# Optimization experiments

Measured on AMD Instinct MI355X. Metric: run time of the kernel, lower is better.

## Reference

```python
import jax, jax.numpy as jnp
import numpy as np

ITERS = 10
EPS = 1e-6
TEMPERATURE = 1.0


def setup_inputs() -> dict:
    key = jax.random.key(0)
    S, E = 524288, 64
    logits = jax.random.normal(key, (S, E), dtype=jnp.float32)
    return {"logits": logits, "top_k": 2}


def reference(logits, top_k):
    s, e = logits.shape
    scores = (logits / TEMPERATURE).astype(jnp.float32)
    scores = scores - jnp.max(scores, axis=-1, keepdims=True)
    q = jnp.exp(scores)
    col_target = float(s) / float(max(e, 1))

    def body(q, _):
        q = q / (jnp.sum(q, axis=1, keepdims=True) + EPS)
        q = q / (jnp.sum(q, axis=0, keepdims=True) + EPS) * col_target
        return q, None

    q, _ = jax.lax.scan(body, q, None, length=ITERS)
    q = q / (jnp.sum(q, axis=1, keepdims=True) + EPS)
    vals, idx = jax.lax.top_k(q, top_k)
    w = vals / (jnp.sum(vals, axis=-1, keepdims=True) + EPS)
    return idx.astype(jnp.int64), w.astype(logits.dtype)
```

## Files before the change

kernel.cpp:

```cpp
#include <hip/hip_runtime.h>
#include <math.h>

#define EPS 1e-6f
#define NE 64
#define THREADS 256
#define WPB 4
#define NBLOCKS 1024
#define ITERS 10

template <int ctrl>
__device__ __forceinline__ float dppf(float x) {
    return __int_as_float(__builtin_amdgcn_update_dpp(
        0, __float_as_int(x), ctrl, 0xf, 0xf, true));
}
template <int ctrl>
__device__ __forceinline__ int dppi(int x) {
    return __builtin_amdgcn_update_dpp(0, x, ctrl, 0xf, 0xf, true);
}

__device__ __forceinline__ float group16_sum(float v) {
    v += dppf<0xB1>(v);
    v += dppf<0x4E>(v);
    v += dppf<0x141>(v);
    v += dppf<0x140>(v);
    return v;
}

#define ARGMAX_STEP(CTRL)                                      \
    {                                                          \
        float ov = dppf<CTRL>(v);                              \
        int oi = dppi<CTRL>(i);                                \
        if (ov > v || (ov == v && oi < i)) { v = ov; i = oi; } \
    }

__device__ __forceinline__ void group16_argmax(float& v, int& i) {
    ARGMAX_STEP(0xB1)
    ARGMAX_STEP(0x4E)
    ARGMAX_STEP(0x141)
    ARGMAX_STEP(0x140)
}

__global__ void sink_init(float* __restrict__ r, float* __restrict__ c, int S) {
    int i = blockIdx.x * blockDim.x + threadIdx.x;
    if (i < S) r[i] = 1.0f;
    if (i < NE) c[i] = 1.0f;
}

__global__ __launch_bounds__(THREADS) void sink_pass(
    const float4* __restrict__ logits4, float* __restrict__ r,
    const float* __restrict__ c, float* __restrict__ Pblk, int nquads) {
    const int lane = threadIdx.x & 63;
    const int wib = threadIdx.x >> 6;
    const int g = lane >> 4;
    const int h = lane & 15;

    const float4 c4 = ((const float4*)c)[h];

    float4 pacc = {0.f, 0.f, 0.f, 0.f};
    int wave = blockIdx.x * WPB + wib;
    int nw = gridDim.x * WPB;

    for (int quad = wave; quad < nquads; quad += nw) {
        float4 v = logits4[(size_t)quad * 64 + lane];
        float4 q;
        q.x = __expf(v.x); q.y = __expf(v.y);
        q.z = __expf(v.z); q.w = __expf(v.w);
        float s = q.x * c4.x + q.y * c4.y + q.z * c4.z + q.w * c4.w;
        s = group16_sum(s);
        int row = quad * 4 + g;
        float rold = r[row];
        float rnew = rold / (rold * s + EPS);
        if (h == 0) r[row] = rnew;
        pacc.x += q.x * rnew; pacc.y += q.y * rnew;
        pacc.z += q.z * rnew; pacc.w += q.w * rnew;
    }

    __shared__ float4 plds[WPB][64];
    plds[wib][lane] = pacc;
    __syncthreads();
    if (threadIdx.x < NE) {
        int j = threadIdx.x;
        int hh = j >> 2, kk = j & 3;
        float t = 0.f;
#pragma unroll
        for (int w = 0; w < WPB; ++w)
#pragma unroll
            for (int gg = 0; gg < 4; ++gg) {
                const float* p = (const float*)&plds[w][gg * 16 + hh];
                t += p[kk];
            }
        Pblk[blockIdx.x * NE + j] = t;
    }
}

__global__ __launch_bounds__(1024) void sink_reduce(
    const float* __restrict__ Pblk, float* __restrict__ c, float col_target) {
    const int j = threadIdx.x & 63;
    const int chunk = threadIdx.x >> 6;
    const int per = NBLOCKS / 16;
    float t = 0.f;
    int b0 = chunk * per;
    for (int b = b0; b < b0 + per; ++b) t += Pblk[b * NE + j];
    __shared__ float lds[16][NE];
    lds[chunk][j] = t;
    __syncthreads();
    if (threadIdx.x < NE) {
        float P = 0.f;
#pragma unroll
        for (int k = 0; k < 16; ++k) P += lds[k][threadIdx.x];
        float cj = c[threadIdx.x];
        c[threadIdx.x] = cj * col_target / (cj * P + EPS);
    }
}

__global__ __launch_bounds__(THREADS) void sink_final(
    const float4* __restrict__ logits4, const float* __restrict__ r,
    const float* __restrict__ c, float2* __restrict__ oidx,
    float2* __restrict__ ow, int nquads) {
    const int lane = threadIdx.x & 63;
    const int wib = threadIdx.x >> 6;
    const int g = lane >> 4;
    const int h = lane & 15;
    const int base_col = h * 4;

    const float4 c4 = ((const float4*)c)[h];

    int wave = blockIdx.x * WPB + wib;
    int nw = gridDim.x * WPB;

    for (int quad = wave; quad < nquads; quad += nw) {
        float4 vv = logits4[(size_t)quad * 64 + lane];
        float4 u;
        u.x = __expf(vv.x) * c4.x; u.y = __expf(vv.y) * c4.y;
        u.z = __expf(vv.z) * c4.z; u.w = __expf(vv.w) * c4.w;
        float s = group16_sum(u.x + u.y + u.z + u.w);
        int row = quad * 4 + g;
        float rold = r[row];
        float rnew = rold / (rold * s + EPS);
        float4 val;
        val.x = u.x * rnew; val.y = u.y * rnew;
        val.z = u.z * rnew; val.w = u.w * rnew;

        float v = val.x; int i = base_col;
        if (val.y > v) { v = val.y; i = base_col + 1; }
        if (val.z > v) { v = val.z; i = base_col + 2; }
        if (val.w > v) { v = val.w; i = base_col + 3; }
        group16_argmax(v, i);
        float v1 = v; int i1 = i;

        float4 mv;
        mv.x = (i1 == base_col)     ? -INFINITY : val.x;
        mv.y = (i1 == base_col + 1) ? -INFINITY : val.y;
        mv.z = (i1 == base_col + 2) ? -INFINITY : val.z;
        mv.w = (i1 == base_col + 3) ? -INFINITY : val.w;
        v = mv.x; i = base_col;
        if (mv.y > v) { v = mv.y; i = base_col + 1; }
        if (mv.z > v) { v = mv.z; i = base_col + 2; }
        if (mv.w > v) { v = mv.w; i = base_col + 3; }
        group16_argmax(v, i);
        float v2 = v; int i2 = i;

        if (h == 0) {
            float wsum = v1 + v2 + EPS;
            oidx[row] = make_float2((float)i1, (float)i2);
            ow[row] = make_float2(v1 / wsum, v2 / wsum);
        }
    }
}

extern "C" void kernel_launch(void* const* d_in, const int* in_sizes, int n_in,
                              void* d_out, int out_size, void* d_ws, size_t ws_size,
                              hipStream_t stream) {
    const float* logits = (const float*)d_in[0];
    const int S = in_sizes[0] / NE;
    const int nquads = S / 4;
    const float col_target = (float)S / (float)NE;

    float* r = (float*)d_ws;
    float* c = r + S;
    float* Pblk = c + NE;

    float* out = (float*)d_out;
    float2* oidx = (float2*)out;
    float2* ow = (float2*)(out + (size_t)2 * S);

    sink_init<<<(S + THREADS - 1) / THREADS, THREADS, 0, stream>>>(r, c, S);
    for (int it = 0; it < ITERS; ++it) {
        sink_pass<<<NBLOCKS, THREADS, 0, stream>>>(
            (const float4*)logits, r, c, Pblk, nquads);
        sink_reduce<<<1, 1024, 0, stream>>>(Pblk, c, col_target);
    }
    sink_final<<<NBLOCKS, THREADS, 0, stream>>>(
        (const float4*)logits, r, c, oidx, ow, nquads);
}
```

Baseline: 602.3 us.

## Fuse Sinkhorn iterations into one persistent cooperative kernel with LDS-resident row scales

Replaces the 22 separate launches (init, pass/reduce per iteration, final) with one cooperative kernel of 256 blocks by 1024 threads. Blocks sync through grid.sync and a double-buffered partial column-sum array. Each wave owns a fixed contiguous range of rows, so the row scale factors stay in shared memory instead of global memory, and the next logits row is software-prefetched. This removes launch gaps and the global traffic for the r vector. In exchange, each block recomputes the 64-column reduction redundantly after every grid sync. It also assumes nquads divides evenly by NBLK*WPB and that each block's rows fit in MAXROWS; it does, since 512 quads per wave times 4 rows gives 2048. With only 256 blocks the logits streaming may get less memory-level parallelism.

```diff
diff --git a/kernel.cpp b/kernel.cpp
--- a/kernel.cpp
+++ b/kernel.cpp
@@ -1,12 +1,16 @@
 #include <hip/hip_runtime.h>
+#include <hip/hip_cooperative_groups.h>
 #include <math.h>
+
+namespace cg = cooperative_groups;
 
 #define EPS 1e-6f
 #define NE 64
-#define THREADS 256
-#define WPB 4
-#define NBLOCKS 1024
+#define NBLK 256
+#define TPB 1024
+#define WPB 16
 #define ITERS 10
+#define MAXROWS 2048
 
 template <int ctrl>
 __device__ __forceinline__ float dppf(float x) {
@@ -40,127 +44,132 @@
     ARGMAX_STEP(0x140)
 }
 
-__global__ void sink_init(float* __restrict__ r, float* __restrict__ c, int S) {
-    int i = blockIdx.x * blockDim.x + threadIdx.x;
-    if (i < S) r[i] = 1.0f;
-    if (i < NE) c[i] = 1.0f;
-}
-
-__global__ __launch_bounds__(THREADS) void sink_pass(
-    const float4* __restrict__ logits4, float* __restrict__ r,
-    const float* __restrict__ c, float* __restrict__ Pblk, int nquads) {
-    const int lane = threadIdx.x & 63;
-    const int wib = threadIdx.x >> 6;
+__global__ __launch_bounds__(TPB, 1) void sink_all(
+    const float4* __restrict__ logits4, float* __restrict__ Pblk,
+    float2* __restrict__ oidx, float2* __restrict__ ow, int nquads,
+    float col_target) {
+    cg::grid_group grid = cg::this_grid();
+    const int tid = threadIdx.x;
+    const int lane = tid & 63;
+    const int wib = tid >> 6;
     const int g = lane >> 4;
     const int h = lane & 15;
+    const int qpw = nquads / (NBLK * WPB);
+    const int qbase = (blockIdx.x * WPB + wib) * qpw;
 
-    const float4 c4 = ((const float4*)c)[h];
+    __shared__ float s_r[MAXROWS];
+    __shared__ float s_c[NE];
+    __shared__ float4 s_pl[WPB][64];
+    float* s_red = (float*)s_pl;
 
-    float4 pacc = {0.f, 0.f, 0.f, 0.f};
-    int wave = blockIdx.x * WPB + wib;
-    int nw = gridDim.x * WPB;
+    for (int i = tid; i < MAXROWS; i += TPB) s_r[i] = 1.0f;
+    if (tid < NE) s_c[tid] = 1.0f;
+    __syncthreads();
 
-    for (int quad = wave; quad < nquads; quad += nw) {
-        float4 v = logits4[(size_t)quad * 64 + lane];
-        float4 q;
-        q.x = __expf(v.x); q.y = __expf(v.y);
-        q.z = __expf(v.z); q.w = __expf(v.w);
-        float s = q.x * c4.x + q.y * c4.y + q.z * c4.z + q.w * c4.w;
-        s = group16_sum(s);
-        int row = quad * 4 + g;
-        float rold = r[row];
-        float rnew = rold / (rold * s + EPS);
-        if (h == 0) r[row] = rnew;
-        pacc.x += q.x * rnew; pacc.y += q.y * rnew;
-        pacc.z += q.z * rnew; pacc.w += q.w * rnew;
+    for (int it = 0; it < ITERS; ++it) {
+        float4 c4;
+        c4.x = s_c[h * 4 + 0]; c4.y = s_c[h * 4 + 1];
+        c4.z = s_c[h * 4 + 2]; c4.w = s_c[h * 4 + 3];
+
+        float4 pacc = {0.f, 0.f, 0.f, 0.f};
+        float4 v = logits4[(size_t)qbase * 64 + lane];
+        for (int k = 0; k < qpw; ++k) {
+            float4 cur = v;
+            if (k + 1 < qpw)
+                v = logits4[(size_t)(qbase + k + 1) * 64 + lane];
+            float4 q;
+            q.x = __expf(cur.x); q.y = __expf(cur.y);
+            q.z = __expf(cur.z); q.w = __expf(cur.w);
+            float s = q.x * c4.x + q.y * c4.y + q.z * c4.z + q.w * c4.w;
+            s = group16_sum(s);
+            int lrow = (wib * qpw + k) * 4 + g;
+            float rold = s_r[lrow];
+            float rnew = rold / (rold * s + EPS);
+            if (h == 0) s_r[lrow] = rnew;
+            pacc.x += q.x * rnew; pacc.y += q.y * rnew;
+            pacc.z += q.z * rnew; pacc.w += q.w * rnew;
+        }
+
+        __syncthreads();
+        s_pl[wib][lane] = pacc;
+        __syncthreads();
+        float* Pout = Pblk + (size_t)(it & 1) * NBLK * NE;
+        if (tid < NE) {
+            int j = tid, hh = j >> 2, kk = j & 3;
+            float t = 0.f;
+#pragma unroll
+            for (int w = 0; w < WPB; ++w)
+#pragma unroll
+                for (int gg = 0; gg < 4; ++gg)
+                    t += ((const float*)&s_pl[w][gg * 16 + hh])[kk];
+            Pout[blockIdx.x * NE + j] = t;
+        }
+        __threadfence();
+        grid.sync();
+
+        const float* Pin = Pblk + (size_t)(it & 1) * NBLK * NE;
+        {
+            int j = tid & 63;
+            int chunk = tid >> 6;
+            float t = 0.f;
+            int b0 = chunk * (NBLK / 16);
+            for (int b = b0; b < b0 + NBLK / 16; ++b) t += Pin[b * NE + j];
+            __syncthreads();
+            s_red[chunk * NE + j] = t;
+            __syncthreads();
+            if (tid < NE) {
+                float P = 0.f;
+#pragma unroll
+                for (int k = 0; k < 16; ++k) P += s_red[k * NE + tid];
+                float cj = s_c[tid];
+                s_c[tid] = cj * col_target / (cj * P + EPS);
+            }
+            __syncthreads();
+        }
     }
 
-    __shared__ float4 plds[WPB][64];
-    plds[wib][lane] = pacc;
-    __syncthreads();
-    if (threadIdx.x < NE) {
-        int j = threadIdx.x;
-        int hh = j >> 2, kk = j & 3;
-        float t = 0.f;
-#pragma unroll
-        for (int w = 0; w < WPB; ++w)
-#pragma unroll
-            for (int gg = 0; gg < 4; ++gg) {
-                const float* p = (const float*)&plds[w][gg * 16 + hh];
-                t += p[kk];
-            }
-        Pblk[blockIdx.x * NE + j] = t;
-    }
-}
-
-__global__ __launch_bounds__(1024) void sink_reduce(
-    const float* __restrict__ Pblk, float* __restrict__ c, float col_target) {
-    const int j = threadIdx.x & 63;
-    const int chunk = threadIdx.x >> 6;
-    const int per = NBLOCKS / 16;
-    float t = 0.f;
-    int b0 = chunk * per;
-    for (int b = b0; b < b0 + per; ++b) t += Pblk[b * NE + j];
-    __shared__ float lds[16][NE];
-    lds[chunk][j] = t;
-    __syncthreads();
-    if (threadIdx.x < NE) {
-        float P = 0.f;
-#pragma unroll
-        for (int k = 0; k < 16; ++k) P += lds[k][threadIdx.x];
-        float cj = c[threadIdx.x];
-        c[threadIdx.x] = cj * col_target / (cj * P + EPS);
-    }
-}
-
-__global__ __launch_bounds__(THREADS) void sink_final(
-    const float4* __restrict__ logits4, const float* __restrict__ r,
-    const float* __restrict__ c, float2* __restrict__ oidx,
-    float2* __restrict__ ow, int nquads) {
-    const int lane = threadIdx.x & 63;
-    const int wib = threadIdx.x >> 6;
-    const int g = lane >> 4;
-    const int h = lane & 15;
+    float4 c4;
+    c4.x = s_c[h * 4 + 0]; c4.y = s_c[h * 4 + 1];
+    c4.z = s_c[h * 4 + 2]; c4.w = s_c[h * 4 + 3];
     const int base_col = h * 4;
 
-    const float4 c4 = ((const float4*)c)[h];
-
-    int wave = blockIdx.x * WPB + wib;
-    int nw = gridDim.x * WPB;
-
-    for (int quad = wave; quad < nquads; quad += nw) {
-        float4 vv = logits4[(size_t)quad * 64 + lane];
+    float4 v = logits4[(size_t)qbase * 64 + lane];
+    for (int k = 0; k < qpw; ++k) {
+        float4 cur = v;
+        if (k + 1 < qpw)
+            v = logits4[(size_t)(qbase + k + 1) * 64 + lane];
         float4 u;
-        u.x = __expf(vv.x) * c4.x; u.y = __expf(vv.y) * c4.y;
-        u.z = __expf(vv.z) * c4.z; u.w = __expf(vv.w) * c4.w;
+        u.x = __expf(cur.x) * c4.x; u.y = __expf(cur.y) * c4.y;
+        u.z = __expf(cur.z) * c4.z; u.w = __expf(cur.w) * c4.w;
         float s = group16_sum(u.x + u.y + u.z + u.w);
-        int row = quad * 4 + g;
-        float rold = r[row];
+        int lrow = (wib * qpw + k) * 4 + g;
+        float rold = s_r[lrow];
         float rnew = rold / (rold * s + EPS);
         float4 val;
         val.x = u.x * rnew; val.y = u.y * rnew;
         val.z = u.z * rnew; val.w = u.w * rnew;
 
-        float v = val.x; int i = base_col;
-        if (val.y > v) { v = val.y; i = base_col + 1; }
-        if (val.z > v) { v = val.z; i = base_col + 2; }
-        if (val.w > v) { v = val.w; i = base_col + 3; }
-        group16_argmax(v, i);
-        float v1 = v; int i1 = i;
+        float vv = val.x; int i = base_col;
+        if (val.y > vv) { vv = val.y; i = base_col + 1; }
+        if (val.z > vv) { vv = val.z; i = base_col + 2; }
+        if (val.w > vv) { vv = val.w; i = base_col + 3; }
+        { float& v = vv; group16_argmax(v, i); }
+        float v1 = vv; int i1 = i;
 
         float4 mv;
         mv.x = (i1 == base_col)     ? -INFINITY : val.x;
         mv.y = (i1 == base_col + 1) ? -INFINITY : val.y;
         mv.z = (i1 == base_col + 2) ? -INFINITY : val.z;
         mv.w = (i1 == base_col + 3) ? -INFINITY : val.w;
-        v = mv.x; i = base_col;
-        if (mv.y > v) { v = mv.y; i = base_col + 1; }
-        if (mv.z > v) { v = mv.z; i = base_col + 2; }
-        if (mv.w > v) { v = mv.w; i = base_col + 3; }
-        group16_argmax(v, i);
-        float v2 = v; int i2 = i;
+        vv = mv.x; i = base_col;
+        if (mv.y > vv) { vv = mv.y; i = base_col + 1; }
+        if (mv.z > vv) { vv = mv.z; i = base_col + 2; }
+        if (mv.w > vv) { vv = mv.w; i = base_col + 3; }
+        { float& v = vv; group16_argmax(v, i); }
+        float v2 = vv; int i2 = i;
 
         if (h == 0) {
+            int row = (qbase + k) * 4 + g;
             float wsum = v1 + v2 + EPS;
             oidx[row] = make_float2((float)i1, (float)i2);
             ow[row] = make_float2(v1 / wsum, v2 / wsum);
@@ -173,23 +182,18 @@
                               hipStream_t stream) {
     const float* logits = (const float*)d_in[0];
     const int S = in_sizes[0] / NE;
-    const int nquads = S / 4;
-    const float col_target = (float)S / (float)NE;
+    int nquads = S / 4;
+    float col_target = (float)S / (float)NE;
 
-    float* r = (float*)d_ws;
-    float* c = r + S;
-    float* Pblk = c + NE;
+    float* Pblk = (float*)d_ws;
 
     float* out = (float*)d_out;
     float2* oidx = (float2*)out;
     float2* ow = (float2*)(out + (size_t)2 * S);
 
-    sink_init<<<(S + THREADS - 1) / THREADS, THREADS, 0, stream>>>(r, c, S);
-    for (int it = 0; it < ITERS; ++it) {
-        sink_pass<<<NBLOCKS, THREADS, 0, stream>>>(
-            (const float4*)logits, r, c, Pblk, nquads);
-        sink_reduce<<<1, 1024, 0, stream>>>(Pblk, c, col_target);
-    }
-    sink_final<<<NBLOCKS, THREADS, 0, stream>>>(
-        (const float4*)logits, r, c, oidx, ow, nquads);
+    const float4* logits4 = (const float4*)logits;
+    void* args[] = {(void*)&logits4, (void*)&Pblk, (void*)&oidx,
+                    (void*)&ow, (void*)&nquads, (void*)&col_target};
+    hipLaunchCooperativeKernel((void*)sink_all, dim3(NBLK), dim3(TPB), args,
+                               0, stream);
 }
```

Result: slower. 1.367 ms (+126.9%).

## Software-prefetch contiguous per-wave chunks and specialize first Sinkhorn pass

Applied to the files above, without the earlier changes.

Each wave now owns a contiguous run of quads instead of a grid-stride loop. Logits and r values are register double-buffered in groups of four quads, so the loads for the next group are in flight while the current group is computed. A templated FIRST pass assumes r and c are all ones, which lets the separate init kernel and the first r/c reads be dropped. The code assumes nquads divides evenly by waves times the prefetch depth, and it uses more registers.

```diff
diff --git a/kernel.cpp b/kernel.cpp
--- a/kernel.cpp
+++ b/kernel.cpp
@@ -6,7 +6,9 @@
 #define THREADS 256
 #define WPB 4
 #define NBLOCKS 1024
+#define NWAVES (NBLOCKS * WPB)
 #define ITERS 10
+#define PF 4
 
 template <int ctrl>
 __device__ __forceinline__ float dppf(float x) {
@@ -40,12 +42,7 @@
     ARGMAX_STEP(0x140)
 }
 
-__global__ void sink_init(float* __restrict__ r, float* __restrict__ c, int S) {
-    int i = blockIdx.x * blockDim.x + threadIdx.x;
-    if (i < S) r[i] = 1.0f;
-    if (i < NE) c[i] = 1.0f;
-}
-
+template <bool FIRST>
 __global__ __launch_bounds__(THREADS) void sink_pass(
     const float4* __restrict__ logits4, float* __restrict__ r,
     const float* __restrict__ c, float* __restrict__ Pblk, int nquads) {
@@ -53,26 +50,58 @@
     const int wib = threadIdx.x >> 6;
     const int g = lane >> 4;
     const int h = lane & 15;
-
-    const float4 c4 = ((const float4*)c)[h];
+    const int qpw = nquads / NWAVES;
+    const int qbase = (blockIdx.x * WPB + wib) * qpw;
+
+    float4 c4;
+    if (FIRST) c4 = make_float4(1.f, 1.f, 1.f, 1.f);
+    else       c4 = ((const float4*)c)[h];
+
+    const float4* lp = logits4 + (size_t)qbase * 64 + lane;
+
+    float4 buf[PF];
+    float rbuf[PF];
+#pragma unroll
+    for (int p = 0; p < PF; ++p) buf[p] = lp[(size_t)p * 64];
+    if (!FIRST) {
+#pragma unroll
+        for (int p = 0; p < PF; ++p) rbuf[p] = r[(qbase + p) * 4 + g];
+    }
 
     float4 pacc = {0.f, 0.f, 0.f, 0.f};
-    int wave = blockIdx.x * WPB + wib;
-    int nw = gridDim.x * WPB;
-
-    for (int quad = wave; quad < nquads; quad += nw) {
-        float4 v = logits4[(size_t)quad * 64 + lane];
-        float4 q;
-        q.x = __expf(v.x); q.y = __expf(v.y);
-        q.z = __expf(v.z); q.w = __expf(v.w);
-        float s = q.x * c4.x + q.y * c4.y + q.z * c4.z + q.w * c4.w;
-        s = group16_sum(s);
-        int row = quad * 4 + g;
-        float rold = r[row];
-        float rnew = rold / (rold * s + EPS);
-        if (h == 0) r[row] = rnew;
-        pacc.x += q.x * rnew; pacc.y += q.y * rnew;
-        pacc.z += q.z * rnew; pacc.w += q.w * rnew;
+    const int nb = qpw / PF;
+    for (int b = 0; b < nb; ++b) {
+        float4 cur[PF];
+        float rcur[PF];
+#pragma unroll
+        for (int p = 0; p < PF; ++p) {
+            cur[p] = buf[p];
+            if (!FIRST) rcur[p] = rbuf[p];
+        }
+        if (b + 1 < nb) {
+            const float4* np = lp + (size_t)(b + 1) * PF * 64;
+#pragma unroll
+            for (int p = 0; p < PF; ++p) buf[p] = np[(size_t)p * 64];
+            if (!FIRST) {
+#pragma unroll
+                for (int p = 0; p < PF; ++p)
+                    rbuf[p] = r[(qbase + (b + 1) * PF + p) * 4 + g];
+            }
+        }
+#pragma unroll
+        for (int p = 0; p < PF; ++p) {
+            float4 q;
+            q.x = __expf(cur[p].x); q.y = __expf(cur[p].y);
+            q.z = __expf(cur[p].z); q.w = __expf(cur[p].w);
+            float s = q.x * c4.x + q.y * c4.y + q.z * c4.z + q.w * c4.w;
+            s = group16_sum(s);
+            float rold = FIRST ? 1.0f : rcur[p];
+            float rnew = rold / (rold * s + EPS);
+            int row = (qbase + b * PF + p) * 4 + g;
+            if (h == 0) r[row] = rnew;
+            pacc.x += q.x * rnew; pacc.y += q.y * rnew;
+            pacc.z += q.z * rnew; pacc.w += q.w * rnew;
+        }
     }
 
     __shared__ float4 plds[WPB][64];
@@ -85,14 +114,13 @@
 #pragma unroll
         for (int w = 0; w < WPB; ++w)
 #pragma unroll
-            for (int gg = 0; gg < 4; ++gg) {
-                const float* p = (const float*)&plds[w][gg * 16 + hh];
-                t += p[kk];
-            }
+            for (int gg = 0; gg < 4; ++gg)
+                t += ((const float*)&plds[w][gg * 16 + hh])[kk];
         Pblk[blockIdx.x * NE + j] = t;
     }
 }
 
+template <bool FIRST>
 __global__ __launch_bounds__(1024) void sink_reduce(
     const float* __restrict__ Pblk, float* __restrict__ c, float col_target) {
     const int j = threadIdx.x & 63;
@@ -108,7 +136,7 @@
         float P = 0.f;
 #pragma unroll
         for (int k = 0; k < 16; ++k) P += lds[k][threadIdx.x];
-        float cj = c[threadIdx.x];
+        float cj = FIRST ? 1.0f : c[threadIdx.x];
         c[threadIdx.x] = cj * col_target / (cj * P + EPS);
     }
 }
@@ -122,48 +150,70 @@
     const int g = lane >> 4;
     const int h = lane & 15;
     const int base_col = h * 4;
+    const int qpw = nquads / NWAVES;
+    const int qbase = (blockIdx.x * WPB + wib) * qpw;
 
     const float4 c4 = ((const float4*)c)[h];
-
-    int wave = blockIdx.x * WPB + wib;
-    int nw = gridDim.x * WPB;
-
-    for (int quad = wave; quad < nquads; quad += nw) {
-        float4 vv = logits4[(size_t)quad * 64 + lane];
-        float4 u;
-        u.x = __expf(vv.x) * c4.x; u.y = __expf(vv.y) * c4.y;
-        u.z = __expf(vv.z) * c4.z; u.w = __expf(vv.w) * c4.w;
-        float s = group16_sum(u.x + u.y + u.z + u.w);
-        int row = quad * 4 + g;
-        float rold = r[row];
-        float rnew = rold / (rold * s + EPS);
-        float4 val;
-        val.x = u.x * rnew; val.y = u.y * rnew;
-        val.z = u.z * rnew; val.w = u.w * rnew;
-
-        float v = val.x; int i = base_col;
-        if (val.y > v) { v = val.y; i = base_col + 1; }
-        if (val.z > v) { v = val.z; i = base_col + 2; }
-        if (val.w > v) { v = val.w; i = base_col + 3; }
-        group16_argmax(v, i);
-        float v1 = v; int i1 = i;
-
-        float4 mv;
-        mv.x = (i1 == base_col)     ? -INFINITY : val.x;
-        mv.y = (i1 == base_col + 1) ? -INFINITY : val.y;
-        mv.z = (i1 == base_col + 2) ? -INFINITY : val.z;
-        mv.w = (i1 == base_col + 3) ? -INFINITY : val.w;
-        v = mv.x; i = base_col;
-        if (mv.y > v) { v = mv.y; i = base_col + 1; }
-        if (mv.z > v) { v = mv.z; i = base_col + 2; }
-        if (mv.w > v) { v = mv.w; i = base_col + 3; }
-        group16_argmax(v, i);
-        float v2 = v; int i2 = i;
-
-        if (h == 0) {
-            float wsum = v1 + v2 + EPS;
-            oidx[row] = make_float2((float)i1, (float)i2);
-            ow[row] = make_float2(v1 / wsum, v2 / wsum);
+    const float4* lp = logits4 + (size_t)qbase * 64 + lane;
+
+    float4 buf[PF];
+    float rbuf[PF];
+#pragma unroll
+    for (int p = 0; p < PF; ++p) buf[p] = lp[(size_t)p * 64];
+#pragma unroll
+    for (int p = 0; p < PF; ++p) rbuf[p] = r[(qbase + p) * 4 + g];
+
+    const int nb = qpw / PF;
+    for (int b = 0; b < nb; ++b) {
+        float4 cur[PF];
+        float rcur[PF];
+#pragma unroll
+        for (int p = 0; p < PF; ++p) { cur[p] = buf[p]; rcur[p] = rbuf[p]; }
+        if (b + 1 < nb) {
+            const float4* np = lp + (size_t)(b + 1) * PF * 64;
+#pragma unroll
+            for (int p = 0; p < PF; ++p) buf[p] = np[(size_t)p * 64];
+#pragma unroll
+            for (int p = 0; p < PF; ++p)
+                rbuf[p] = r[(qbase + (b + 1) * PF + p) * 4 + g];
+        }
+#pragma unroll
+        for (int p = 0; p < PF; ++p) {
+            float4 u;
+            u.x = __expf(cur[p].x) * c4.x; u.y = __expf(cur[p].y) * c4.y;
+            u.z = __expf(cur[p].z) * c4.z; u.w = __expf(cur[p].w) * c4.w;
+            float s = group16_sum(u.x + u.y + u.z + u.w);
+            float rold = rcur[p];
+            float rnew = rold / (rold * s + EPS);
+            float4 val;
+            val.x = u.x * rnew; val.y = u.y * rnew;
+            val.z = u.z * rnew; val.w = u.w * rnew;
+
+            float v = val.x; int i = base_col;
+            if (val.y > v) { v = val.y; i = base_col + 1; }
+            if (val.z > v) { v = val.z; i = base_col + 2; }
+            if (val.w > v) { v = val.w; i = base_col + 3; }
+            group16_argmax(v, i);
+            float v1 = v; int i1 = i;
+
+            float4 mv;
+            mv.x = (i1 == base_col)     ? -INFINITY : val.x;
+            mv.y = (i1 == base_col + 1) ? -INFINITY : val.y;
+            mv.z = (i1 == base_col + 2) ? -INFINITY : val.z;
+            mv.w = (i1 == base_col + 3) ? -INFINITY : val.w;
+            v = mv.x; i = base_col;
+            if (mv.y > v) { v = mv.y; i = base_col + 1; }
+            if (mv.z > v) { v = mv.z; i = base_col + 2; }
+            if (mv.w > v) { v = mv.w; i = base_col + 3; }
+            group16_argmax(v, i);
+            float v2 = v; int i2 = i;
+
+            if (h == 0) {
+                int row = (qbase + b * PF + p) * 4 + g;
+                float wsum = v1 + v2 + EPS;
+                oidx[row] = make_float2((float)i1, (float)i2);
+                ow[row] = make_float2(v1 / wsum, v2 / wsum);
+            }
         }
     }
 }
@@ -184,12 +234,13 @@
     float2* oidx = (float2*)out;
     float2* ow = (float2*)(out + (size_t)2 * S);
 
-    sink_init<<<(S + THREADS - 1) / THREADS, THREADS, 0, stream>>>(r, c, S);
-    for (int it = 0; it < ITERS; ++it) {
-        sink_pass<<<NBLOCKS, THREADS, 0, stream>>>(
-            (const float4*)logits, r, c, Pblk, nquads);
-        sink_reduce<<<1, 1024, 0, stream>>>(Pblk, c, col_target);
-    }
-    sink_final<<<NBLOCKS, THREADS, 0, stream>>>(
-        (const float4*)logits, r, c, oidx, ow, nquads);
-}
+    const float4* l4 = (const float4*)logits;
+
+    sink_pass<true><<<NBLOCKS, THREADS, 0, stream>>>(l4, r, c, Pblk, nquads);
+    sink_reduce<true><<<1, 1024, 0, stream>>>(Pblk, c, col_target);
+    for (int it = 1; it < ITERS; ++it) {
+        sink_pass<false><<<NBLOCKS, THREADS, 0, stream>>>(l4, r, c, Pblk, nquads);
+        sink_reduce<false><<<1, 1024, 0, stream>>>(Pblk, c, col_target);
+    }
+    sink_final<<<NBLOCKS, THREADS, 0, stream>>>(l4, r, c, oidx, ow, nquads);
+}
```

Result: no change. 614.0 us (+1.9%).
